# Kernel optimization log

Measured on AMD Instinct MI355X. Metric: run time of the kernel, lower is better.

## Reference

```python
import jax, jax.numpy as jnp
import numpy as np

N_NODES = 50000
N_EDGES = 800000
IN_F = 128
OUT_F = 128
N_LAYERS = 2


def setup_inputs() -> dict:
    key = jax.random.key(0)
    ks = jax.random.split(key, 8)
    x = jax.random.normal(ks[0], (N_NODES, IN_F), dtype=jnp.float32)
    hidden_states = jax.random.normal(ks[1], (N_LAYERS, N_NODES, OUT_F), dtype=jnp.float32)
    src = jax.random.randint(ks[2], (N_EDGES,), 0, N_NODES)
    dst = jax.random.randint(ks[3], (N_EDGES,), 0, N_NODES)
    edge_w = jax.random.uniform(ks[4], (N_EDGES,), dtype=jnp.float32)
    # [layer, gate(r,u,c), in+out, out], scaled like typical init
    W_self = jax.random.normal(ks[5], (N_LAYERS, 3, IN_F + OUT_F, OUT_F), dtype=jnp.float32) * 0.05
    W_neigh = jax.random.normal(ks[6], (N_LAYERS, 3, IN_F + OUT_F, OUT_F), dtype=jnp.float32) * 0.05
    bias = jax.random.uniform(ks[7], (N_LAYERS, 3, OUT_F), dtype=jnp.float32)
    return {"x": x, "hidden_states": hidden_states, "src": src, "dst": dst,
            "edge_w": edge_w, "W_self": W_self, "W_neigh": W_neigh, "bias": bias}


def _gconv(z, src, dst, edge_w, ws, wn):
    # z: [N, 2F]; message passing: sum_{e: dst=v} edge_w[e] * z[src[e]]
    msg = z[src] * edge_w[:, None]                      # [E, 2F]
    agg = jax.ops.segment_sum(msg, dst, num_segments=N_NODES)  # [N, 2F]
    return z @ ws + agg @ wn                            # [N, F]


def _cell(x, h, src, dst, edge_w, ws, wn, b):
    # ws/wn: [3, 2F, F], b: [3, F]; gates r,u,c as in GraphGRUCell
    xh = jnp.concatenate([x, h], axis=1)
    r = jax.nn.sigmoid(_gconv(xh, src, dst, edge_w, ws[0], wn[0]) + b[0])
    u = jax.nn.sigmoid(_gconv(xh, src, dst, edge_w, ws[1], wn[1]) + b[1])
    xh2 = jnp.concatenate([x, r * h], axis=1)
    c = jax.nn.sigmoid(_gconv(xh2, src, dst, edge_w, ws[2], wn[2]) + b[2])
    return u * h + (1.0 - u) * c


def reference(x, hidden_states, src, dst, edge_w, W_self, W_neigh, bias):
    hiddens = []
    for i in range(N_LAYERS):  # small fixed layer count
        x = _cell(x, hidden_states[i], src, dst, edge_w, W_self[i], W_neigh[i], bias[i])
        hiddens.append(x)
    return (x, hiddens)
```

## Files before the change

kernel.cpp:

```cpp
#include <hip/hip_runtime.h>
#include <math.h>

#define F 128
#define NLAYERS 2

typedef __attribute__((ext_vector_type(8))) short bf16x8s;
typedef __attribute__((ext_vector_type(4))) float f32x4;

__device__ __forceinline__ float sigmoidf_(float x) { return 1.0f / (1.0f + expf(-x)); }

__device__ __forceinline__ unsigned short f2bf(float f) {
    unsigned int u = __float_as_uint(f);
    u += 0x7fffu + ((u >> 16) & 1u);
    return (unsigned short)(u >> 16);
}
__device__ __forceinline__ float bf2f(unsigned short s) {
    return __uint_as_float(((unsigned int)s) << 16);
}

__global__ void pack_w_bf16(const float* __restrict__ Ws, const float* __restrict__ Wn,
                            unsigned short* __restrict__ W1b, unsigned short* __restrict__ W2b) {
    int t = blockIdx.x * blockDim.x + threadIdx.x;
    const int n1 = 2 * 64 * 256 * 8;
    if (t < n1) {
        int j = t & 7, n = (t >> 3) & 255, ko = (t >> 11) & 63, l = t >> 17;
        int k = ko * 8 + j;
        int p = k >> 7, r = k & 127, g = n >> 7, c = n & 127;
        const float* W = (p < 2) ? Ws : Wn;
        W1b[t] = f2bf(W[(((l * 3 + g) * 256) + ((p & 1) * 128 + r)) * 128 + c]);
    } else {
        int t2 = t - n1;
        if (t2 >= 2 * 64 * 128 * 8) return;
        int j = t2 & 7, n = (t2 >> 3) & 127, ko = (t2 >> 10) & 63, l = t2 >> 16;
        int k = ko * 8 + j;
        int p = k >> 7, r = k & 127;
        const float* W = (p < 2) ? Ws : Wn;
        W2b[t2] = f2bf(W[(((l * 3 + 2) * 256) + ((p & 1) * 128 + r)) * 128 + n]);
    }
}

__global__ void cvt_bf16(const float* __restrict__ in, unsigned short* __restrict__ out, int n4) {
    int t = blockIdx.x * blockDim.x + threadIdx.x;
    if (t >= n4) return;
    float4 v = reinterpret_cast<const float4*>(in)[t];
    ushort4 o;
    o.x = f2bf(v.x); o.y = f2bf(v.y); o.z = f2bf(v.z); o.w = f2bf(v.w);
    reinterpret_cast<ushort4*>(out)[t] = o;
}

__global__ void hist_dst(const int* __restrict__ dst, int* __restrict__ cnt, int E) {
    int e = blockIdx.x * blockDim.x + threadIdx.x;
    if (e < E) atomicAdd(&cnt[dst[e]], 1);
}

__global__ __launch_bounds__(1024) void scan_offs(const int* __restrict__ cnt,
                                                  int* __restrict__ offs,
                                                  int* __restrict__ cursor, int n) {
    __shared__ int wsum[16];
    __shared__ int carry_s;
    int tid = threadIdx.x;
    int lane = tid & 63, wid = tid >> 6;
    if (tid == 0) carry_s = 0;
    __syncthreads();
    for (int base = 0; base < n; base += 1024) {
        int i = base + tid;
        int v = (i < n) ? cnt[i] : 0;
        int incl = v;
#pragma unroll
        for (int off = 1; off < 64; off <<= 1) {
            int t = __shfl_up(incl, off, 64);
            if (lane >= off) incl += t;
        }
        if (lane == 63) wsum[wid] = incl;
        __syncthreads();
        if (wid == 0) {
            int s = (lane < 16) ? wsum[lane] : 0;
#pragma unroll
            for (int off = 1; off < 16; off <<= 1) {
                int t = __shfl_up(s, off, 64);
                if (lane >= off) s += t;
            }
            if (lane < 16) wsum[lane] = s;
        }
        __syncthreads();
        int wbase = (wid > 0) ? wsum[wid - 1] : 0;
        int carry = carry_s;
        int excl = carry + wbase + incl - v;
        if (i < n) { offs[i] = excl; cursor[i] = excl; }
        __syncthreads();
        if (tid == 1023) carry_s = carry + wsum[15];
        __syncthreads();
    }
    if (threadIdx.x == 0) offs[n] = carry_s;
}

__global__ void scatter_edges(const int* __restrict__ src, const int* __restrict__ dst,
                              const float* __restrict__ ew, int* __restrict__ cursor,
                              int2* __restrict__ es, int E) {
    int e = blockIdx.x * blockDim.x + threadIdx.x;
    if (e >= E) return;
    int d = dst[e];
    int p = atomicAdd(&cursor[d], 1);
    es[p] = make_int2(src[e], __float_as_int(ew[e]));
}

__global__ __launch_bounds__(256) void agg_csr2_b(
    const unsigned short* __restrict__ V0, const unsigned short* __restrict__ V1,
    const int2* __restrict__ es, const int* __restrict__ offs,
    unsigned short* __restrict__ agg0, unsigned short* __restrict__ agg1, int N) {
    int node = blockIdx.x * 8 + (threadIdx.x >> 5);
    if (node >= N) return;
    int lane = threadIdx.x & 31;
    int beg = offs[node], end = offs[node + 1];
    float p0[4] = {0, 0, 0, 0}, q0[4] = {0, 0, 0, 0};
    float p1[4] = {0, 0, 0, 0}, q1[4] = {0, 0, 0, 0};
    int i = beg;
    for (; i + 1 < end; i += 2) {
        int2 e0 = es[i], e1 = es[i + 1];
        float w0 = __int_as_float(e0.y), w1 = __int_as_float(e1.y);
        size_t r0 = ((size_t)e0.x << 7) + (lane << 2);
        size_t r1 = ((size_t)e1.x << 7) + (lane << 2);
        ushort4 x0 = *reinterpret_cast<const ushort4*>(V0 + r0);
        ushort4 x1 = *reinterpret_cast<const ushort4*>(V0 + r1);
        ushort4 h0 = *reinterpret_cast<const ushort4*>(V1 + r0);
        ushort4 h1 = *reinterpret_cast<const ushort4*>(V1 + r1);
        p0[0] += w0 * bf2f(x0.x); p0[1] += w0 * bf2f(x0.y);
        p0[2] += w0 * bf2f(x0.z); p0[3] += w0 * bf2f(x0.w);
        p1[0] += w1 * bf2f(x1.x); p1[1] += w1 * bf2f(x1.y);
        p1[2] += w1 * bf2f(x1.z); p1[3] += w1 * bf2f(x1.w);
        q0[0] += w0 * bf2f(h0.x); q0[1] += w0 * bf2f(h0.y);
        q0[2] += w0 * bf2f(h0.z); q0[3] += w0 * bf2f(h0.w);
        q1[0] += w1 * bf2f(h1.x); q1[1] += w1 * bf2f(h1.y);
        q1[2] += w1 * bf2f(h1.z); q1[3] += w1 * bf2f(h1.w);
    }
    if (i < end) {
        int2 e0 = es[i];
        float w0 = __int_as_float(e0.y);
        size_t r0 = ((size_t)e0.x << 7) + (lane << 2);
        ushort4 x0 = *reinterpret_cast<const ushort4*>(V0 + r0);
        ushort4 h0 = *reinterpret_cast<const ushort4*>(V1 + r0);
        p0[0] += w0 * bf2f(x0.x); p0[1] += w0 * bf2f(x0.y);
        p0[2] += w0 * bf2f(x0.z); p0[3] += w0 * bf2f(x0.w);
        q0[0] += w0 * bf2f(h0.x); q0[1] += w0 * bf2f(h0.y);
        q0[2] += w0 * bf2f(h0.z); q0[3] += w0 * bf2f(h0.w);
    }
    size_t ob = ((size_t)node << 7) + (lane << 2);
    ushort4 o0, o1;
    o0.x = f2bf(p0[0] + p1[0]); o0.y = f2bf(p0[1] + p1[1]);
    o0.z = f2bf(p0[2] + p1[2]); o0.w = f2bf(p0[3] + p1[3]);
    o1.x = f2bf(q0[0] + q1[0]); o1.y = f2bf(q0[1] + q1[1]);
    o1.z = f2bf(q0[2] + q1[2]); o1.w = f2bf(q0[3] + q1[3]);
    *reinterpret_cast<ushort4*>(agg0 + ob) = o0;
    *reinterpret_cast<ushort4*>(agg1 + ob) = o1;
}

__global__ __launch_bounds__(256) void agg_csr1_b(
    const unsigned short* __restrict__ V0,
    const int2* __restrict__ es, const int* __restrict__ offs,
    unsigned short* __restrict__ agg0, int N) {
    int node = blockIdx.x * 8 + (threadIdx.x >> 5);
    if (node >= N) return;
    int lane = threadIdx.x & 31;
    int beg = offs[node], end = offs[node + 1];
    float p0[4] = {0, 0, 0, 0}, p1[4] = {0, 0, 0, 0};
    int i = beg;
    for (; i + 1 < end; i += 2) {
        int2 e0 = es[i], e1 = es[i + 1];
        float w0 = __int_as_float(e0.y), w1 = __int_as_float(e1.y);
        size_t r0 = ((size_t)e0.x << 7) + (lane << 2);
        size_t r1 = ((size_t)e1.x << 7) + (lane << 2);
        ushort4 x0 = *reinterpret_cast<const ushort4*>(V0 + r0);
        ushort4 x1 = *reinterpret_cast<const ushort4*>(V0 + r1);
        p0[0] += w0 * bf2f(x0.x); p0[1] += w0 * bf2f(x0.y);
        p0[2] += w0 * bf2f(x0.z); p0[3] += w0 * bf2f(x0.w);
        p1[0] += w1 * bf2f(x1.x); p1[1] += w1 * bf2f(x1.y);
        p1[2] += w1 * bf2f(x1.z); p1[3] += w1 * bf2f(x1.w);
    }
    if (i < end) {
        int2 e0 = es[i];
        float w0 = __int_as_float(e0.y);
        size_t r0 = ((size_t)e0.x << 7) + (lane << 2);
        ushort4 x0 = *reinterpret_cast<const ushort4*>(V0 + r0);
        p0[0] += w0 * bf2f(x0.x); p0[1] += w0 * bf2f(x0.y);
        p0[2] += w0 * bf2f(x0.z); p0[3] += w0 * bf2f(x0.w);
    }
    size_t ob = ((size_t)node << 7) + (lane << 2);
    ushort4 o0;
    o0.x = f2bf(p0[0] + p1[0]); o0.y = f2bf(p0[1] + p1[1]);
    o0.z = f2bf(p0[2] + p1[2]); o0.w = f2bf(p0[3] + p1[3]);
    *reinterpret_cast<ushort4*>(agg0 + ob) = o0;
}

__global__ __launch_bounds__(256) void gemm_mfma(
    const unsigned short* __restrict__ A0, const unsigned short* __restrict__ A1,
    const unsigned short* __restrict__ A2, const unsigned short* __restrict__ A3,
    const unsigned short* __restrict__ Wb, const float* __restrict__ bias,
    const float* __restrict__ hfull, const float* __restrict__ uin,
    unsigned short* __restrict__ outb, float* __restrict__ outf,
    float* __restrict__ outf2, int Nn, int Ntot, int mode) {
    __shared__ __align__(16) unsigned short Als[2][4 * 64 * 8];
    __shared__ __align__(16) unsigned short Bls[2][4 * 128 * 8];
    const unsigned short* parts[4] = {A0, A1, A2, A3};

    int tid = threadIdx.x;
    int row0 = blockIdx.x * 64;
    int n0c = blockIdx.y * 128;
    int lane = tid & 63;
    int w = tid >> 6;
    int wrow = (w & 1) << 5;
    int wcol = (w >> 1) << 6;
    int quad = lane >> 4, l16 = lane & 15;

    f32x4 acc[2][4];
    const f32x4 z4 = {0.f, 0.f, 0.f, 0.f};
#pragma unroll
    for (int mt = 0; mt < 2; ++mt)
#pragma unroll
        for (int nt = 0; nt < 4; ++nt) acc[mt][nt] = z4;

    int growA = row0 + lane;
    if (growA >= Nn) growA = Nn - 1;
    int qB = tid >> 7, nB = tid & 127;

    auto stage = [&](int ks, int buf) {
        const unsigned short* ga = parts[ks >> 7] + ((size_t)growA << 7) + (ks & 127) + (w << 3);
        __builtin_amdgcn_global_load_lds(
            (const __attribute__((address_space(1))) void*)ga,
            (__attribute__((address_space(3))) void*)&Als[buf][((w << 6) + lane) << 3], 16, 0, 0);
#pragma unroll
        for (int r = 0; r < 2; ++r) {
            int q = 2 * r + qB;
            int koG = (ks >> 3) + q;
            const unsigned short* gb = Wb + ((size_t)(koG * Ntot + n0c + nB) << 3);
            __builtin_amdgcn_global_load_lds(
                (const __attribute__((address_space(1))) void*)gb,
                (__attribute__((address_space(3))) void*)&Bls[buf][((q << 7) + nB) << 3], 16, 0, 0);
        }
    };

    stage(0, 0);
    __syncthreads();
    int buf = 0;
    for (int ks = 0; ks < 512; ks += 32, buf ^= 1) {
        if (ks + 32 < 512) stage(ks + 32, buf ^ 1);

        bf16x8s af[2], bfr[4];
#pragma unroll
        for (int mt = 0; mt < 2; ++mt)
            af[mt] = *reinterpret_cast<const bf16x8s*>(
                &Als[buf][((quad << 6) + wrow + (mt << 4) + l16) << 3]);
#pragma unroll
        for (int nt = 0; nt < 4; ++nt)
            bfr[nt] = *reinterpret_cast<const bf16x8s*>(
                &Bls[buf][((quad << 7) + wcol + (nt << 4) + l16) << 3]);
#pragma unroll
        for (int mt = 0; mt < 2; ++mt)
#pragma unroll
            for (int nt = 0; nt < 4; ++nt)
                acc[mt][nt] = __builtin_amdgcn_mfma_f32_16x16x32_bf16(
                    af[mt], bfr[nt], acc[mt][nt], 0, 0, 0);
        __syncthreads();
    }

#pragma unroll
    for (int mt = 0; mt < 2; ++mt) {
#pragma unroll
        for (int reg = 0; reg < 4; ++reg) {
            int row = row0 + wrow + (mt << 4) + (quad << 2) + reg;
            if (row >= Nn) continue;
#pragma unroll
            for (int nt = 0; nt < 4; ++nt) {
                int col = n0c + wcol + (nt << 4) + l16;
                float val = acc[mt][nt][reg] + bias[col];
                if (mode == 0) {
                    float sg = sigmoidf_(val);
                    int c = col & 127;
                    size_t o = ((size_t)row << 7) + c;
                    if (col < 128)
                        outb[o] = f2bf(sg * hfull[o]);
                    else
                        outf[o] = sg;
                } else {
                    float cv = sigmoidf_(val);
                    size_t o = ((size_t)row << 7) + col;
                    float uu = uin[o];
                    float hh = hfull[o];
                    float hn = uu * hh + (1.0f - uu) * cv;
                    outf[o] = hn;
                    if (outf2) outf2[o] = hn;
                    outb[o] = f2bf(hn);
                }
            }
        }
    }
}

extern "C" void kernel_launch(void* const* d_in, const int* in_sizes, int n_in,
                              void* d_out, int out_size, void* d_ws, size_t ws_size,
                              hipStream_t stream) {
    const float* x      = (const float*)d_in[0];
    const float* hidden = (const float*)d_in[1];
    const int*   src    = (const int*)d_in[2];
    const int*   dst    = (const int*)d_in[3];
    const float* ew     = (const float*)d_in[4];
    const float* Wself  = (const float*)d_in[5];
    const float* Wneigh = (const float*)d_in[6];
    const float* bias   = (const float*)d_in[7];
    float* out = (float*)d_out;

    int N = in_sizes[0] / F;
    int E = in_sizes[2];
    size_t NF = (size_t)N * F;

    char* p = (char*)d_ws;
    auto alloc = [&](size_t bytes) { char* r = p; p += (bytes + 255) & ~255ull; return r; };
    unsigned short* xb0    = (unsigned short*)alloc(NF * 2);
    unsigned short* xb1    = (unsigned short*)alloc(NF * 2);
    unsigned short* hb     = (unsigned short*)alloc(2 * NF * 2);
    unsigned short* agg_xb = (unsigned short*)alloc(NF * 2);
    unsigned short* agg_hb = (unsigned short*)alloc(NF * 2);
    unsigned short* agg_rb = (unsigned short*)alloc(NF * 2);
    unsigned short* rhb    = (unsigned short*)alloc(NF * 2);
    float*          u      = (float*)alloc(NF * 4);
    unsigned short* W1b    = (unsigned short*)alloc(2 * 64 * 256 * 8 * 2);
    unsigned short* W2b    = (unsigned short*)alloc(2 * 64 * 128 * 8 * 2);
    int2*           es     = (int2*)alloc((size_t)E * 8);
    int*            cnt    = (int*)alloc((size_t)N * 4);
    int*            offs   = (int*)alloc(((size_t)N + 1) * 4);
    int*            cursor = (int*)alloc((size_t)N * 4);

    pack_w_bf16<<<dim3(1536), dim3(256), 0, stream>>>(Wself, Wneigh, W1b, W2b);
    cvt_bf16<<<dim3((int)(NF / 4 + 255) / 256, 1), dim3(256), 0, stream>>>(x, xb0, (int)(NF / 4));
    cvt_bf16<<<dim3((int)(2 * NF / 4 + 255) / 256, 1), dim3(256), 0, stream>>>(hidden, hb, (int)(2 * NF / 4));

    hipMemsetAsync(cnt, 0, (size_t)N * sizeof(int), stream);
    int eBlocks = (E + 255) / 256;
    hist_dst<<<dim3(eBlocks), dim3(256), 0, stream>>>(dst, cnt, E);
    scan_offs<<<dim3(1), dim3(1024), 0, stream>>>(cnt, offs, cursor, N);
    scatter_edges<<<dim3(eBlocks), dim3(256), 0, stream>>>(src, dst, ew, cursor, es, E);

    float* out_x  = out;
    float* out_h1 = out + NF;
    float* out_h2 = out + 2 * NF;

    int aggBlocks = (N + 7) / 8;
    int mBlocks = (N + 63) / 64;
    for (int l = 0; l < NLAYERS; ++l) {
        const unsigned short* xbL = (l == 0) ? xb0 : xb1;
        const unsigned short* hbL = hb + (size_t)l * NF;
        const float* hL = hidden + (size_t)l * NF;
        const float* biasL = bias + (size_t)l * 384;

        agg_csr2_b<<<dim3(aggBlocks), dim3(256), 0, stream>>>(xbL, hbL, es, offs,
                                                              agg_xb, agg_hb, N);

        gemm_mfma<<<dim3(mBlocks, 2), dim3(256), 0, stream>>>(
            xbL, hbL, agg_xb, agg_hb,
            W1b + (size_t)l * 64 * 256 * 8, biasL, hL, nullptr,
            rhb, u, nullptr, N, 256, 0);

        agg_csr1_b<<<dim3(aggBlocks), dim3(256), 0, stream>>>(rhb, es, offs, agg_rb, N);

        float* o1 = (l == 0) ? out_h1 : out_h2;
        float* o2 = (l == NLAYERS - 1) ? out_x : nullptr;
        unsigned short* xbN = (l == 0) ? xb1 : xb0;
        gemm_mfma<<<dim3(mBlocks, 1), dim3(256), 0, stream>>>(
            xbL, rhb, agg_xb, agg_rb,
            W2b + (size_t)l * 64 * 128 * 8, biasL + 256, hL, u,
            xbN, o1, o2, N, 128, 1);
    }
}
```

Baseline: 666.0 us.

## Interleave x and h bf16 rows and parallelize the CSR offset scan

Stores the bf16 x and hidden features for each node together in one 256-wide row. Each edge gather in the two-input aggregation then reads one contiguous 512-byte row with 16-byte loads instead of two separate rows. The GEMM gets stride arguments so it can read the interleaved layout and write the next layer's x into it. The single-block serial scan is replaced by a three-kernel block scan, and both aggregation kernels now unroll by four edges. Costs are extra kernel launches, and the last layer writes its unused bf16 output into a buffer that the same GEMM also reads, which depends on each block touching only its own rows.

```diff
diff --git a/kernel.cpp b/kernel.cpp
--- a/kernel.cpp
+++ b/kernel.cpp
@@ -5,6 +5,7 @@
 #define NLAYERS 2
 
 typedef __attribute__((ext_vector_type(8))) short bf16x8s;
+typedef __attribute__((ext_vector_type(8))) unsigned short u16x8;
 typedef __attribute__((ext_vector_type(4))) float f32x4;
 
 __device__ __forceinline__ float sigmoidf_(float x) { return 1.0f / (1.0f + expf(-x)); }
@@ -39,13 +40,13 @@
     }
 }
 
-__global__ void cvt_bf16(const float* __restrict__ in, unsigned short* __restrict__ out, int n4) {
+__global__ void cvt_bf16_i(const float* __restrict__ in, unsigned short* __restrict__ out, int n4) {
     int t = blockIdx.x * blockDim.x + threadIdx.x;
     if (t >= n4) return;
     float4 v = reinterpret_cast<const float4*>(in)[t];
     ushort4 o;
     o.x = f2bf(v.x); o.y = f2bf(v.y); o.z = f2bf(v.z); o.w = f2bf(v.w);
-    reinterpret_cast<ushort4*>(out)[t] = o;
+    *reinterpret_cast<ushort4*>(out + (((size_t)(t >> 5)) << 8) + ((t & 31) << 2)) = o;
 }
 
 __global__ void hist_dst(const int* __restrict__ dst, int* __restrict__ cnt, int E) {
@@ -53,45 +54,72 @@
     if (e < E) atomicAdd(&cnt[dst[e]], 1);
 }
 
-__global__ __launch_bounds__(1024) void scan_offs(const int* __restrict__ cnt,
-                                                  int* __restrict__ offs,
-                                                  int* __restrict__ cursor, int n) {
+__global__ __launch_bounds__(1024) void scan_blk(const int* __restrict__ cnt,
+                                                 int* __restrict__ offs,
+                                                 int* __restrict__ bsum, int n) {
     __shared__ int wsum[16];
-    __shared__ int carry_s;
-    int tid = threadIdx.x;
-    int lane = tid & 63, wid = tid >> 6;
-    if (tid == 0) carry_s = 0;
+    int tid = threadIdx.x, lane = tid & 63, wid = tid >> 6;
+    int i = blockIdx.x * 1024 + tid;
+    int v = (i < n) ? cnt[i] : 0;
+    int incl = v;
+#pragma unroll
+    for (int off = 1; off < 64; off <<= 1) {
+        int t = __shfl_up(incl, off, 64);
+        if (lane >= off) incl += t;
+    }
+    if (lane == 63) wsum[wid] = incl;
     __syncthreads();
-    for (int base = 0; base < n; base += 1024) {
-        int i = base + tid;
-        int v = (i < n) ? cnt[i] : 0;
-        int incl = v;
-#pragma unroll
-        for (int off = 1; off < 64; off <<= 1) {
-            int t = __shfl_up(incl, off, 64);
-            if (lane >= off) incl += t;
+    if (wid == 0) {
+        int s = (lane < 16) ? wsum[lane] : 0;
+#pragma unroll
+        for (int off = 1; off < 16; off <<= 1) {
+            int t = __shfl_up(s, off, 64);
+            if (lane >= off) s += t;
         }
-        if (lane == 63) wsum[wid] = incl;
-        __syncthreads();
-        if (wid == 0) {
-            int s = (lane < 16) ? wsum[lane] : 0;
-#pragma unroll
-            for (int off = 1; off < 16; off <<= 1) {
-                int t = __shfl_up(s, off, 64);
-                if (lane >= off) s += t;
-            }
-            if (lane < 16) wsum[lane] = s;
+        if (lane < 16) wsum[lane] = s;
+    }
+    __syncthreads();
+    int wbase = (wid > 0) ? wsum[wid - 1] : 0;
+    if (i < n) offs[i] = wbase + incl - v;
+    if (tid == 1023) bsum[blockIdx.x] = wbase + incl;
+}
+
+__global__ __launch_bounds__(1024) void scan_tops(int* __restrict__ bsum, int nb,
+                                                  int* __restrict__ total_out) {
+    __shared__ int wsum[16];
+    int tid = threadIdx.x, lane = tid & 63, wid = tid >> 6;
+    int v = (tid < nb) ? bsum[tid] : 0;
+    int incl = v;
+#pragma unroll
+    for (int off = 1; off < 64; off <<= 1) {
+        int t = __shfl_up(incl, off, 64);
+        if (lane >= off) incl += t;
+    }
+    if (lane == 63) wsum[wid] = incl;
+    __syncthreads();
+    if (wid == 0) {
+        int s = (lane < 16) ? wsum[lane] : 0;
+#pragma unroll
+        for (int off = 1; off < 16; off <<= 1) {
+            int t = __shfl_up(s, off, 64);
+            if (lane >= off) s += t;
         }
-        __syncthreads();
-        int wbase = (wid > 0) ? wsum[wid - 1] : 0;
-        int carry = carry_s;
-        int excl = carry + wbase + incl - v;
-        if (i < n) { offs[i] = excl; cursor[i] = excl; }
-        __syncthreads();
-        if (tid == 1023) carry_s = carry + wsum[15];
-        __syncthreads();
-    }
-    if (threadIdx.x == 0) offs[n] = carry_s;
+        if (lane < 16) wsum[lane] = s;
+    }
+    __syncthreads();
+    int wbase = (wid > 0) ? wsum[wid - 1] : 0;
+    if (tid < nb) bsum[tid] = wbase + incl - v;
+    if (tid == 1023) *total_out = wbase + incl;
+}
+
+__global__ __launch_bounds__(1024) void scan_add(const int* __restrict__ bsum,
+                                                 int* __restrict__ offs,
+                                                 int* __restrict__ cursor, int n) {
+    int i = blockIdx.x * 1024 + threadIdx.x;
+    if (i >= n) return;
+    int o = offs[i] + bsum[blockIdx.x];
+    offs[i] = o;
+    cursor[i] = o;
 }
 
 __global__ void scatter_edges(const int* __restrict__ src, const int* __restrict__ dst,
@@ -104,54 +132,48 @@
     es[p] = make_int2(src[e], __float_as_int(ew[e]));
 }
 
-__global__ __launch_bounds__(256) void agg_csr2_b(
-    const unsigned short* __restrict__ V0, const unsigned short* __restrict__ V1,
+__global__ __launch_bounds__(256) void agg_csr2_i(
+    const unsigned short* __restrict__ XH,
     const int2* __restrict__ es, const int* __restrict__ offs,
     unsigned short* __restrict__ agg0, unsigned short* __restrict__ agg1, int N) {
     int node = blockIdx.x * 8 + (threadIdx.x >> 5);
     if (node >= N) return;
     int lane = threadIdx.x & 31;
     int beg = offs[node], end = offs[node + 1];
-    float p0[4] = {0, 0, 0, 0}, q0[4] = {0, 0, 0, 0};
-    float p1[4] = {0, 0, 0, 0}, q1[4] = {0, 0, 0, 0};
+    float a0[8] = {0, 0, 0, 0, 0, 0, 0, 0};
+    float a1[8] = {0, 0, 0, 0, 0, 0, 0, 0};
+    int loff = lane << 3;
     int i = beg;
-    for (; i + 1 < end; i += 2) {
-        int2 e0 = es[i], e1 = es[i + 1];
+    for (; i + 3 < end; i += 4) {
+        int2 e0 = es[i], e1 = es[i + 1], e2 = es[i + 2], e3 = es[i + 3];
+        u16x8 v0 = *reinterpret_cast<const u16x8*>(XH + (((size_t)e0.x) << 8) + loff);
+        u16x8 v1 = *reinterpret_cast<const u16x8*>(XH + (((size_t)e1.x) << 8) + loff);
+        u16x8 v2 = *reinterpret_cast<const u16x8*>(XH + (((size_t)e2.x) << 8) + loff);
+        u16x8 v3 = *reinterpret_cast<const u16x8*>(XH + (((size_t)e3.x) << 8) + loff);
         float w0 = __int_as_float(e0.y), w1 = __int_as_float(e1.y);
-        size_t r0 = ((size_t)e0.x << 7) + (lane << 2);
-        size_t r1 = ((size_t)e1.x << 7) + (lane << 2);
-        ushort4 x0 = *reinterpret_cast<const ushort4*>(V0 + r0);
-        ushort4 x1 = *reinterpret_cast<const ushort4*>(V0 + r1);
-        ushort4 h0 = *reinterpret_cast<const ushort4*>(V1 + r0);
-        ushort4 h1 = *reinterpret_cast<const ushort4*>(V1 + r1);
-        p0[0] += w0 * bf2f(x0.x); p0[1] += w0 * bf2f(x0.y);
-        p0[2] += w0 * bf2f(x0.z); p0[3] += w0 * bf2f(x0.w);
-        p1[0] += w1 * bf2f(x1.x); p1[1] += w1 * bf2f(x1.y);
-        p1[2] += w1 * bf2f(x1.z); p1[3] += w1 * bf2f(x1.w);
-        q0[0] += w0 * bf2f(h0.x); q0[1] += w0 * bf2f(h0.y);
-        q0[2] += w0 * bf2f(h0.z); q0[3] += w0 * bf2f(h0.w);
-        q1[0] += w1 * bf2f(h1.x); q1[1] += w1 * bf2f(h1.y);
-        q1[2] += w1 * bf2f(h1.z); q1[3] += w1 * bf2f(h1.w);
-    }
-    if (i < end) {
+        float w2 = __int_as_float(e2.y), w3 = __int_as_float(e3.y);
+#pragma unroll
+        for (int j = 0; j < 8; ++j) {
+            a0[j] += w0 * bf2f(v0[j]);
+            a1[j] += w1 * bf2f(v1[j]);
+            a0[j] += w2 * bf2f(v2[j]);
+            a1[j] += w3 * bf2f(v3[j]);
+        }
+    }
+    for (; i < end; ++i) {
         int2 e0 = es[i];
         float w0 = __int_as_float(e0.y);
-        size_t r0 = ((size_t)e0.x << 7) + (lane << 2);
-        ushort4 x0 = *reinterpret_cast<const ushort4*>(V0 + r0);
-        ushort4 h0 = *reinterpret_cast<const ushort4*>(V1 + r0);
-        p0[0] += w0 * bf2f(x0.x); p0[1] += w0 * bf2f(x0.y);
-        p0[2] += w0 * bf2f(x0.z); p0[3] += w0 * bf2f(x0.w);
-        q0[0] += w0 * bf2f(h0.x); q0[1] += w0 * bf2f(h0.y);
-        q0[2] += w0 * bf2f(h0.z); q0[3] += w0 * bf2f(h0.w);
-    }
-    size_t ob = ((size_t)node << 7) + (lane << 2);
-    ushort4 o0, o1;
-    o0.x = f2bf(p0[0] + p1[0]); o0.y = f2bf(p0[1] + p1[1]);
-    o0.z = f2bf(p0[2] + p1[2]); o0.w = f2bf(p0[3] + p1[3]);
-    o1.x = f2bf(q0[0] + q1[0]); o1.y = f2bf(q0[1] + q1[1]);
-    o1.z = f2bf(q0[2] + q1[2]); o1.w = f2bf(q0[3] + q1[3]);
-    *reinterpret_cast<ushort4*>(agg0 + ob) = o0;
-    *reinterpret_cast<ushort4*>(agg1 + ob) = o1;
+        u16x8 v0 = *reinterpret_cast<const u16x8*>(XH + (((size_t)e0.x) << 8) + loff);
+#pragma unroll
+        for (int j = 0; j < 8; ++j) a0[j] += w0 * bf2f(v0[j]);
+    }
+    u16x8 o;
+#pragma unroll
+    for (int j = 0; j < 8; ++j) o[j] = f2bf(a0[j] + a1[j]);
+    unsigned short* op = (lane < 16)
+        ? (agg0 + (((size_t)node) << 7) + (lane << 3))
+        : (agg1 + (((size_t)node) << 7) + ((lane & 15) << 3));
+    *reinterpret_cast<u16x8*>(op) = o;
 }
 
 __global__ __launch_bounds__(256) void agg_csr1_b(
@@ -163,28 +185,33 @@
     int lane = threadIdx.x & 31;
     int beg = offs[node], end = offs[node + 1];
     float p0[4] = {0, 0, 0, 0}, p1[4] = {0, 0, 0, 0};
+    int loff = lane << 2;
     int i = beg;
-    for (; i + 1 < end; i += 2) {
-        int2 e0 = es[i], e1 = es[i + 1];
+    for (; i + 3 < end; i += 4) {
+        int2 e0 = es[i], e1 = es[i + 1], e2 = es[i + 2], e3 = es[i + 3];
+        ushort4 x0 = *reinterpret_cast<const ushort4*>(V0 + (((size_t)e0.x) << 7) + loff);
+        ushort4 x1 = *reinterpret_cast<const ushort4*>(V0 + (((size_t)e1.x) << 7) + loff);
+        ushort4 x2 = *reinterpret_cast<const ushort4*>(V0 + (((size_t)e2.x) << 7) + loff);
+        ushort4 x3 = *reinterpret_cast<const ushort4*>(V0 + (((size_t)e3.x) << 7) + loff);
         float w0 = __int_as_float(e0.y), w1 = __int_as_float(e1.y);
-        size_t r0 = ((size_t)e0.x << 7) + (lane << 2);
-        size_t r1 = ((size_t)e1.x << 7) + (lane << 2);
-        ushort4 x0 = *reinterpret_cast<const ushort4*>(V0 + r0);
-        ushort4 x1 = *reinterpret_cast<const ushort4*>(V0 + r1);
+        float w2 = __int_as_float(e2.y), w3 = __int_as_float(e3.y);
         p0[0] += w0 * bf2f(x0.x); p0[1] += w0 * bf2f(x0.y);
         p0[2] += w0 * bf2f(x0.z); p0[3] += w0 * bf2f(x0.w);
         p1[0] += w1 * bf2f(x1.x); p1[1] += w1 * bf2f(x1.y);
         p1[2] += w1 * bf2f(x1.z); p1[3] += w1 * bf2f(x1.w);
-    }
-    if (i < end) {
+        p0[0] += w2 * bf2f(x2.x); p0[1] += w2 * bf2f(x2.y);
+        p0[2] += w2 * bf2f(x2.z); p0[3] += w2 * bf2f(x2.w);
+        p1[0] += w3 * bf2f(x3.x); p1[1] += w3 * bf2f(x3.y);
+        p1[2] += w3 * bf2f(x3.z); p1[3] += w3 * bf2f(x3.w);
+    }
+    for (; i < end; ++i) {
         int2 e0 = es[i];
         float w0 = __int_as_float(e0.y);
-        size_t r0 = ((size_t)e0.x << 7) + (lane << 2);
-        ushort4 x0 = *reinterpret_cast<const ushort4*>(V0 + r0);
+        ushort4 x0 = *reinterpret_cast<const ushort4*>(V0 + (((size_t)e0.x) << 7) + loff);
         p0[0] += w0 * bf2f(x0.x); p0[1] += w0 * bf2f(x0.y);
         p0[2] += w0 * bf2f(x0.z); p0[3] += w0 * bf2f(x0.w);
     }
-    size_t ob = ((size_t)node << 7) + (lane << 2);
+    size_t ob = (((size_t)node) << 7) + loff;
     ushort4 o0;
     o0.x = f2bf(p0[0] + p1[0]); o0.y = f2bf(p0[1] + p1[1]);
     o0.z = f2bf(p0[2] + p1[2]); o0.w = f2bf(p0[3] + p1[3]);
@@ -194,6 +221,7 @@
 __global__ __launch_bounds__(256) void gemm_mfma(
     const unsigned short* __restrict__ A0, const unsigned short* __restrict__ A1,
     const unsigned short* __restrict__ A2, const unsigned short* __restrict__ A3,
+    int sA0, int sA1, int obsh,
     const unsigned short* __restrict__ Wb, const float* __restrict__ bias,
     const float* __restrict__ hfull, const float* __restrict__ uin,
     unsigned short* __restrict__ outb, float* __restrict__ outf,
@@ -223,7 +251,11 @@
     int qB = tid >> 7, nB = tid & 127;
 
     auto stage = [&](int ks, int buf) {
-        const unsigned short* ga = parts[ks >> 7] + ((size_t)growA << 7) + (ks & 127) + (w << 3);
+        int p = ks >> 7;
+        size_t roff = (p == 0) ? (size_t)growA * (size_t)sA0
+                    : (p == 1) ? (size_t)growA * (size_t)sA1
+                               : ((size_t)growA << 7);
+        const unsigned short* ga = parts[p] + roff + (ks & 127) + (w << 3);
         __builtin_amdgcn_global_load_lds(
             (const __attribute__((address_space(1))) void*)ga,
             (__attribute__((address_space(3))) void*)&Als[buf][((w << 6) + lane) << 3], 16, 0, 0);
@@ -288,7 +320,7 @@
                     float hn = uu * hh + (1.0f - uu) * cv;
                     outf[o] = hn;
                     if (outf2) outf2[o] = hn;
-                    outb[o] = f2bf(hn);
+                    outb[((size_t)row << obsh) + col] = f2bf(hn);
                 }
             }
         }
@@ -314,9 +346,8 @@
 
     char* p = (char*)d_ws;
     auto alloc = [&](size_t bytes) { char* r = p; p += (bytes + 255) & ~255ull; return r; };
-    unsigned short* xb0    = (unsigned short*)alloc(NF * 2);
-    unsigned short* xb1    = (unsigned short*)alloc(NF * 2);
-    unsigned short* hb     = (unsigned short*)alloc(2 * NF * 2);
+    unsigned short* xh0    = (unsigned short*)alloc(2 * NF * 2);
+    unsigned short* xh1    = (unsigned short*)alloc(2 * NF * 2);
     unsigned short* agg_xb = (unsigned short*)alloc(NF * 2);
     unsigned short* agg_hb = (unsigned short*)alloc(NF * 2);
     unsigned short* agg_rb = (unsigned short*)alloc(NF * 2);
@@ -328,15 +359,22 @@
     int*            cnt    = (int*)alloc((size_t)N * 4);
     int*            offs   = (int*)alloc(((size_t)N + 1) * 4);
     int*            cursor = (int*)alloc((size_t)N * 4);
+    int*            bsum   = (int*)alloc(1024 * 4);
 
     pack_w_bf16<<<dim3(1536), dim3(256), 0, stream>>>(Wself, Wneigh, W1b, W2b);
-    cvt_bf16<<<dim3((int)(NF / 4 + 255) / 256, 1), dim3(256), 0, stream>>>(x, xb0, (int)(NF / 4));
-    cvt_bf16<<<dim3((int)(2 * NF / 4 + 255) / 256, 1), dim3(256), 0, stream>>>(hidden, hb, (int)(2 * NF / 4));
+    int n4 = (int)(NF / 4);
+    int cblk = (n4 + 255) / 256;
+    cvt_bf16_i<<<dim3(cblk), dim3(256), 0, stream>>>(x, xh0, n4);
+    cvt_bf16_i<<<dim3(cblk), dim3(256), 0, stream>>>(hidden, xh0 + 128, n4);
+    cvt_bf16_i<<<dim3(cblk), dim3(256), 0, stream>>>(hidden + NF, xh1 + 128, n4);
 
     hipMemsetAsync(cnt, 0, (size_t)N * sizeof(int), stream);
     int eBlocks = (E + 255) / 256;
     hist_dst<<<dim3(eBlocks), dim3(256), 0, stream>>>(dst, cnt, E);
-    scan_offs<<<dim3(1), dim3(1024), 0, stream>>>(cnt, offs, cursor, N);
+    int nb = (N + 1023) / 1024;
+    scan_blk<<<dim3(nb), dim3(1024), 0, stream>>>(cnt, offs, bsum, N);
+    scan_tops<<<dim3(1), dim3(1024), 0, stream>>>(bsum, nb, offs + N);
+    scan_add<<<dim3(nb), dim3(1024), 0, stream>>>(bsum, offs, cursor, N);
     scatter_edges<<<dim3(eBlocks), dim3(256), 0, stream>>>(src, dst, ew, cursor, es, E);
 
     float* out_x  = out;
@@ -346,16 +384,15 @@
     int aggBlocks = (N + 7) / 8;
     int mBlocks = (N + 63) / 64;
     for (int l = 0; l < NLAYERS; ++l) {
-        const unsigned short* xbL = (l == 0) ? xb0 : xb1;
-        const unsigned short* hbL = hb + (size_t)l * NF;
+        unsigned short* xhL = (l == 0) ? xh0 : xh1;
         const float* hL = hidden + (size_t)l * NF;
         const float* biasL = bias + (size_t)l * 384;
 
-        agg_csr2_b<<<dim3(aggBlocks), dim3(256), 0, stream>>>(xbL, hbL, es, offs,
+        agg_csr2_i<<<dim3(aggBlocks), dim3(256), 0, stream>>>(xhL, es, offs,
                                                               agg_xb, agg_hb, N);
 
         gemm_mfma<<<dim3(mBlocks, 2), dim3(256), 0, stream>>>(
-            xbL, hbL, agg_xb, agg_hb,
+            xhL, xhL + 128, agg_xb, agg_hb, 256, 256, 7,
             W1b + (size_t)l * 64 * 256 * 8, biasL, hL, nullptr,
             rhb, u, nullptr, N, 256, 0);
 
@@ -363,10 +400,11 @@
 
         float* o1 = (l == 0) ? out_h1 : out_h2;
         float* o2 = (l == NLAYERS - 1) ? out_x : nullptr;
-        unsigned short* xbN = (l == 0) ? xb1 : xb0;
+        unsigned short* obN = (l == 0) ? xh1 : agg_rb;
+        int obsh = (l == 0) ? 8 : 7;
         gemm_mfma<<<dim3(mBlocks, 1), dim3(256), 0, stream>>>(
-            xbL, rhb, agg_xb, agg_rb,
+            xhL, rhb, agg_xb, agg_rb, 256, 128, obsh,
             W2b + (size_t)l * 64 * 128 * 8, biasL + 256, hL, u,
-            xbN, o1, o2, N, 128, 1);
-    }
-}
+            obN, o1, o2, N, 128, 1);
+    }
+}
```

Result: faster. 608.5 us (-8.6%).
